# Kernel tuning notes

Hardware: AMD Instinct MI355X
Metric: run time of the kernel (lower is better)

## Reference

```python
import jax, jax.numpy as jnp
import numpy as np

N = 100000      # nodes per protein batch
E = 1600000     # edges per protein batch
F = 128         # num_features_pro
D = 128         # output_dim
B = 128         # number of graphs in the batch
NEG_SLOPE = 0.01  # nn.LeakyReLU default


def setup_inputs() -> dict:
    key = jax.random.key(0)
    ks = jax.random.split(key, 16)
    inp = {}
    inp["pro1_x"] = jax.random.normal(ks[0], (N, F), dtype=jnp.float32)
    inp["pro2_x"] = jax.random.normal(ks[1], (N, F), dtype=jnp.float32)
    inp["pro1_edge_index"] = jax.random.randint(ks[2], (2, E), 0, N, dtype=jnp.int64 if jax.config.jax_enable_x64 else jnp.int32)
    inp["pro2_edge_index"] = jax.random.randint(ks[3], (2, E), 0, N, dtype=jnp.int64 if jax.config.jax_enable_x64 else jnp.int32)
    inp["pro1_batch"] = jnp.sort(jax.random.randint(ks[4], (N,), 0, B))
    inp["pro2_batch"] = jnp.sort(jax.random.randint(ks[5], (N,), 0, B))
    s = 1.0 / np.sqrt(F)
    inp["conv1_W"] = jax.random.uniform(ks[6], (F, D), minval=-s, maxval=s)
    inp["conv1_b"] = jnp.zeros((D,), jnp.float32)
    inp["conv2_W"] = jax.random.uniform(ks[7], (F, D), minval=-s, maxval=s)
    inp["conv2_b"] = jnp.zeros((D,), jnp.float32)
    sd = 1.0 / np.sqrt(D)
    inp["fc_p1_W"] = jax.random.uniform(ks[8], (D, D), minval=-sd, maxval=sd)
    inp["fc_p1_b"] = jax.random.uniform(ks[9], (D,), minval=-sd, maxval=sd)
    inp["fc_p2_W"] = jax.random.uniform(ks[10], (D, D), minval=-sd, maxval=sd)
    inp["fc_p2_b"] = jax.random.uniform(ks[11], (D,), minval=-sd, maxval=sd)
    s1 = 1.0 / np.sqrt(2 * D)
    inp["fc1_W"] = jax.random.uniform(ks[12], (2 * D, 256), minval=-s1, maxval=s1)
    inp["fc1_b"] = jnp.zeros((256,), jnp.float32)
    s2 = 1.0 / np.sqrt(256)
    inp["fc2_W"] = jax.random.uniform(ks[13], (256, 64), minval=-s2, maxval=s2)
    inp["fc2_b"] = jnp.zeros((64,), jnp.float32)
    s3 = 1.0 / np.sqrt(64)
    inp["out_W"] = jax.random.uniform(ks[14], (64, 1), minval=-s3, maxval=s3)
    inp["out_b"] = jnp.zeros((1,), jnp.float32)
    return inp


def lrelu(x):
    return jnp.where(x >= 0, x, NEG_SLOPE * x)


def gcn_conv(x, edge_index, W, b):
    n = x.shape[0]
    xw = x @ W  # [N, D]
    loop = jnp.arange(n, dtype=edge_index.dtype)
    row = jnp.concatenate([edge_index[0], loop])  # sources
    col = jnp.concatenate([edge_index[1], loop])  # destinations
    deg = jax.ops.segment_sum(jnp.ones_like(col, dtype=xw.dtype), col, num_segments=n)
    dinv = jnp.where(deg > 0, jax.lax.rsqrt(deg), 0.0)
    norm = dinv[row] * dinv[col]  # [E+N]
    msg = norm[:, None] * xw[row]  # gather + scale
    return jax.ops.segment_sum(msg, col, num_segments=n) + b


def branch(x, edge_index, batch, conv_W, conv_b, fc_W, fc_b):
    h = lrelu(gcn_conv(x, edge_index, conv_W, conv_b))
    g = jax.ops.segment_max(h, batch, num_segments=B)  # global max pool -> [B, D]
    return lrelu(g @ fc_W + fc_b)  # dropout is identity at eval


def reference(pro1_x, pro1_edge_index, pro1_batch, pro2_x, pro2_edge_index, pro2_batch,
              conv1_W, conv1_b, conv2_W, conv2_b, fc_p1_W, fc_p1_b, fc_p2_W, fc_p2_b,
              fc1_W, fc1_b, fc2_W, fc2_b, out_W, out_b):
    g1 = branch(pro1_x, pro1_edge_index, pro1_batch, conv1_W, conv1_b, fc_p1_W, fc_p1_b)
    g2 = branch(pro2_x, pro2_edge_index, pro2_batch, conv2_W, conv2_b, fc_p2_W, fc_p2_b)
    c = jnp.concatenate([g1, g2], axis=1)  # [B, 2D]
    c = lrelu(c @ fc1_W + fc1_b)
    c = lrelu(c @ fc2_W + fc2_b)
    return jax.nn.sigmoid(c @ out_W + out_b)  # [B, 1]
```

## Files before the change

### kernel.cpp

```cpp
#include <hip/hip_runtime.h>
#include <math.h>

#define NSLOPE 0.01f
#define BGRAPH 128
#define GTILE 128
#define PNB 512
#define MAXBUK 2048
#define SCAP 4608
#define SCHUNK 6400

typedef unsigned int uv4 __attribute__((ext_vector_type(4)));
typedef short bf16x8 __attribute__((ext_vector_type(8)));
typedef float f32x4 __attribute__((ext_vector_type(4)));

__device__ __forceinline__ float lrelu(float v) { return v >= 0.f ? v : NSLOPE * v; }

__device__ __forceinline__ unsigned fkey(float v) {
  v = v + 0.0f;
  unsigned b = __float_as_uint(v);
  return (b & 0x80000000u) ? ~b : (b | 0x80000000u);
}
__device__ __forceinline__ float fdec(unsigned k) {
  return __uint_as_float((k & 0x80000000u) ? (k ^ 0x80000000u) : ~k);
}
__device__ __forceinline__ unsigned bf16rne(float f) {
  unsigned b = __float_as_uint(f);
  return (b + 0x7fffu + ((b >> 16) & 1u)) >> 16;
}
__device__ __forceinline__ void bfunpack8(uint4 w, float4& lo, float4& hi) {
  lo.x = __uint_as_float(w.x << 16); lo.y = __uint_as_float(w.x & 0xffff0000u);
  lo.z = __uint_as_float(w.y << 16); lo.w = __uint_as_float(w.y & 0xffff0000u);
  hi.x = __uint_as_float(w.z << 16); hi.y = __uint_as_float(w.z & 0xffff0000u);
  hi.z = __uint_as_float(w.w << 16); hi.w = __uint_as_float(w.w & 0xffff0000u);
}
__device__ __forceinline__ void add8(float4& alo, float4& ahi, const float4 lo, const float4 hi) {
  alo.x += lo.x; alo.y += lo.y; alo.z += lo.z; alo.w += lo.w;
  ahi.x += hi.x; ahi.y += hi.y; ahi.z += hi.z; ahi.w += hi.w;
}

__global__ __launch_bounds__(1024) void partition_kernel(
    const int* __restrict__ s1, const int* __restrict__ d1,
    const int* __restrict__ s2, const int* __restrict__ d2,
    int* __restrict__ cnt, int* __restrict__ ebuf,
    int ne, int off, int nbuk) {
  __shared__ int h[MAXBUK];
  __shared__ int lbase[MAXBUK + 1];
  __shared__ int cur[MAXBUK];
  __shared__ int sorted[SCHUNK];
  __shared__ int sscan[1024];
  int t = threadIdx.x;
  for (int i = t; i < nbuk; i += 1024) h[i] = 0;
  __syncthreads();
  int total = 2 * ne;
  int chunk = (total + gridDim.x - 1) / gridDim.x;
  int a = blockIdx.x * chunk;
  int b = min(total, a + chunk);
  int m = b - a;
  for (int e = a + t; e < b; e += 1024) {
    int d = (e < ne) ? d1[e] : d2[e - ne] + off;
    atomicAdd(&h[d >> 7], 1);
  }
  __syncthreads();
  int a0 = (2 * t < nbuk) ? h[2 * t] : 0;
  int a1 = (2 * t + 1 < nbuk) ? h[2 * t + 1] : 0;
  int ps = a0 + a1;
  sscan[t] = ps;
  __syncthreads();
  for (int o = 1; o < 1024; o <<= 1) {
    int u = (t >= o) ? sscan[t - o] : 0;
    __syncthreads();
    sscan[t] += u;
    __syncthreads();
  }
  int excl = sscan[t] - ps;
  if (2 * t < nbuk) { lbase[2 * t] = excl; cur[2 * t] = excl; }
  if (2 * t + 1 < nbuk) { lbase[2 * t + 1] = excl + a0; cur[2 * t + 1] = excl + a0; }
  if (t == 0) lbase[nbuk] = sscan[1023];
  __syncthreads();
  for (int i = t; i < nbuk; i += 1024) {
    int hv = h[i];
    if (hv) h[i] = i * SCAP + atomicAdd(&cnt[i], hv) - lbase[i];
  }
  __syncthreads();
  for (int e = a + t; e < b; e += 1024) {
    int s, d;
    if (e < ne) { s = s1[e]; d = d1[e]; }
    else { s = s2[e - ne] + off; d = d2[e - ne] + off; }
    int bk = d >> 7;
    int p = atomicAdd(&cur[bk], 1);
    sorted[p] = (s << 7) | (d & 127);
  }
  __syncthreads();
  for (int i = t; i < m; i += 1024) {
    int lo = 0, hi = nbuk - 1;
    while (lo < hi) {
      int mid = (lo + hi + 1) >> 1;
      if (lbase[mid] <= i) lo = mid; else hi = mid - 1;
    }
    ebuf[h[lo] + i] = sorted[i];
  }
}

__global__ __launch_bounds__(256) void bucket_sort_kernel(
    int* __restrict__ ebuf, const int* __restrict__ cnt,
    int* __restrict__ rowptr, int* __restrict__ rowend, float* __restrict__ dinv,
    const float* __restrict__ x1, const float* __restrict__ x2,
    uint2* __restrict__ xh,
    const float* __restrict__ W1, const float* __restrict__ W2,
    unsigned short* __restrict__ Wt1, unsigned short* __restrict__ Wt2,
    unsigned* __restrict__ gbuf, int n1, int ntot) {
  __shared__ int buf[SCAP];
  __shared__ int outv[SCAP];
  __shared__ int h[128];
  __shared__ int sc[128];
  __shared__ int cur[128];
  __shared__ float sdv[128];
  int b = blockIdx.x, t = threadIdx.x;
  if (b < 64) {
    int idx = b * 256 + t;
    int k = idx >> 7, n = idx & 127;
    Wt1[n * 128 + k] = (unsigned short)bf16rne(W1[idx]);
    Wt2[n * 128 + k] = (unsigned short)bf16rne(W2[idx]);
  }
  if (b < 128) gbuf[b * 256 + t] = 0u;
  int v0 = b * 128;
  int e0 = b * SCAP;
  int cntb = cnt[b];
  if (t < 128) h[t] = 0;
  for (int i = t; i < cntb; i += 256) buf[i] = ebuf[e0 + i];
  __syncthreads();
  for (int i = t; i < cntb; i += 256) atomicAdd(&h[buf[i] & 127], 1);
  __syncthreads();
  if (t < 128) sc[t] = h[t];
  __syncthreads();
  for (int off = 1; off < 128; off <<= 1) {
    int u = (t < 128 && t >= off) ? sc[t - off] : 0;
    __syncthreads();
    if (t < 128) sc[t] += u;
    __syncthreads();
  }
  if (t < 128) {
    int excl = sc[t] - h[t];
    cur[t] = excl;
    float dv = rsqrtf((float)(h[t] + 1));
    sdv[t] = dv;
    int v = v0 + t;
    if (v < ntot) {
      rowptr[v] = e0 + excl;
      rowend[v] = e0 + excl + h[t];
      dinv[v] = dv;
    }
  }
  __syncthreads();
  for (int i = t; i < cntb; i += 256) {
    int p = buf[i];
    int pos = atomicAdd(&cur[p & 127], 1);
    outv[pos] = p >> 7;
  }
  __syncthreads();
  for (int i = t; i < cntb; i += 256) ebuf[e0 + i] = outv[i];
  for (int i = t; i < 128 * 32; i += 256) {
    int nl = i >> 5, l = i & 31;
    int v = v0 + nl;
    if (v >= ntot) break;
    const float4* xr = (v < n1) ? (const float4*)(x1 + (size_t)v * 128)
                                : (const float4*)(x2 + (size_t)(v - n1) * 128);
    float4 xv = xr[l];
    float dv = sdv[nl];
    unsigned b0 = bf16rne(dv * xv.x), b1 = bf16rne(dv * xv.y);
    unsigned b2 = bf16rne(dv * xv.z), b3 = bf16rne(dv * xv.w);
    uint2 w;
    w.x = (b1 << 16) | b0;
    w.y = (b3 << 16) | b2;
    xh[(size_t)v * 32 + l] = w;
  }
}

__global__ __launch_bounds__(256) void gather_kernel(
    const uint4* __restrict__ xh, const int* __restrict__ csr,
    const int* __restrict__ rowptr, const int* __restrict__ rowend,
    const float* __restrict__ dinv,
    uv4* __restrict__ agg16, int vbase, int vlimit) {
  int tid = blockIdx.x * blockDim.x + threadIdx.x;
  int v = vbase + (tid >> 4), l = tid & 15;
  if (v >= vlimit) return;
  float4 a0, a1, b0, b1;
  bfunpack8(xh[(size_t)v * 16 + l], a0, a1);
  b0 = make_float4(0.f, 0.f, 0.f, 0.f); b1 = b0;
  int rs = __builtin_nontemporal_load(&rowptr[v]);
  int re = __builtin_nontemporal_load(&rowend[v]);
  float dv = dinv[v];
  int base = rs;
  int idx0 = rs + l;
  int sown = (idx0 < re) ? __builtin_nontemporal_load(&csr[idx0]) : 0;

#define LD(slot, j) w##slot = xh[(size_t)__shfl(sown, (j), 16) * 16 + l]
#define UP(slot, p0, p1) { float4 lo_, hi_; bfunpack8(w##slot, lo_, hi_); add8(p0, p1, lo_, hi_); }

  for (; base + 16 <= re; base += 16) {
    int nidx = base + 16 + l;
    int snext = (nidx < re) ? __builtin_nontemporal_load(&csr[nidx]) : 0;
    uint4 w0, w1, w2, w3, w4, w5, w6, w7;
    LD(0, 0); LD(1, 1); LD(2, 2); LD(3, 3);
    LD(4, 4); LD(5, 5); LD(6, 6); LD(7, 7);
    UP(0, a0, a1); LD(0, 8);
    UP(1, b0, b1); LD(1, 9);
    UP(2, a0, a1); LD(2, 10);
    UP(3, b0, b1); LD(3, 11);
    UP(4, a0, a1); LD(4, 12);
    UP(5, b0, b1); LD(5, 13);
    UP(6, a0, a1); LD(6, 14);
    UP(7, b0, b1); LD(7, 15);
    UP(0, a0, a1); UP(1, b0, b1); UP(2, a0, a1); UP(3, b0, b1);
    UP(4, a0, a1); UP(5, b0, b1); UP(6, a0, a1); UP(7, b0, b1);
    sown = snext;
  }
  int m = re - base;
  if (m >= 8) {
    uint4 w0, w1, w2, w3, w4, w5, w6, w7;
    LD(0, 0); LD(1, 1); LD(2, 2); LD(3, 3);
    LD(4, 4); LD(5, 5); LD(6, 6); LD(7, 7);
    UP(0, a0, a1); UP(1, b0, b1); UP(2, a0, a1); UP(3, b0, b1);
    UP(4, a0, a1); UP(5, b0, b1); UP(6, a0, a1); UP(7, b0, b1);
  }
  int jb = m & 8;
  int rem = m & 7;
  if (rem) {
    uint4 t0, t1, t2, t3, t4, t5, t6;
    if (rem > 0) t0 = xh[(size_t)__shfl(sown, jb + 0, 16) * 16 + l];
    if (rem > 1) t1 = xh[(size_t)__shfl(sown, jb + 1, 16) * 16 + l];
    if (rem > 2) t2 = xh[(size_t)__shfl(sown, jb + 2, 16) * 16 + l];
    if (rem > 3) t3 = xh[(size_t)__shfl(sown, jb + 3, 16) * 16 + l];
    if (rem > 4) t4 = xh[(size_t)__shfl(sown, jb + 4, 16) * 16 + l];
    if (rem > 5) t5 = xh[(size_t)__shfl(sown, jb + 5, 16) * 16 + l];
    if (rem > 6) t6 = xh[(size_t)__shfl(sown, jb + 6, 16) * 16 + l];
    float4 lo, hi;
    if (rem > 0) { bfunpack8(t0, lo, hi); add8(a0, a1, lo, hi); }
    if (rem > 1) { bfunpack8(t1, lo, hi); add8(b0, b1, lo, hi); }
    if (rem > 2) { bfunpack8(t2, lo, hi); add8(a0, a1, lo, hi); }
    if (rem > 3) { bfunpack8(t3, lo, hi); add8(b0, b1, lo, hi); }
    if (rem > 4) { bfunpack8(t4, lo, hi); add8(a0, a1, lo, hi); }
    if (rem > 5) { bfunpack8(t5, lo, hi); add8(b0, b1, lo, hi); }
    if (rem > 6) { bfunpack8(t6, lo, hi); add8(a0, a1, lo, hi); }
  }
#undef LD
#undef UP

  add8(a0, a1, b0, b1);
  uv4 w;
  w.x = (bf16rne(dv * a0.y) << 16) | bf16rne(dv * a0.x);
  w.y = (bf16rne(dv * a0.w) << 16) | bf16rne(dv * a0.z);
  w.z = (bf16rne(dv * a1.y) << 16) | bf16rne(dv * a1.x);
  w.w = (bf16rne(dv * a1.w) << 16) | bf16rne(dv * a1.z);
  __builtin_nontemporal_store(w, &agg16[(size_t)v * 16 + l]);
}

__global__ __launch_bounds__(256) void gemm_mfma_pool_kernel(
    const bf16x8* __restrict__ A8,
    const bf16x8* __restrict__ Wt1, const float* __restrict__ b1,
    const bf16x8* __restrict__ Wt2, const float* __restrict__ b2,
    const int* __restrict__ batch1, const int* __restrict__ batch2,
    unsigned* __restrict__ gbuf, int N1, int Ntot, int nbA) {
  __shared__ int sgid[128];
  __shared__ unsigned lmax[8 * 128];
  __shared__ int s_span;
  int b = blockIdx.x;
  int half = (b >= nbA) ? 1 : 0;
  const bf16x8* Wt = half ? Wt2 : Wt1;
  const float* bias = half ? b2 : b1;
  int base = half ? (N1 + (b - nbA) * GTILE) : b * GTILE;
  int rmax = half ? Ntot : N1;
  int t = threadIdx.x;
  int w = t >> 6, lane = t & 63;
  int quad = lane >> 4, lr = lane & 15;

  if (t < 128) {
    int gr = base + t;
    int gid = -1;
    if (gr < rmax) gid = half ? (BGRAPH + batch2[gr - N1]) : batch1[gr];
    sgid[t] = gid;
  }
  for (int i = t; i < 8 * 128; i += 256) lmax[i] = 0u;
  __syncthreads();
  int g0 = sgid[0];
  if (t == 0) {
    int mg = g0;
    for (int r = 127; r >= 0; r--) {
      if (sgid[r] >= 0) { mg = sgid[r]; break; }
    }
    s_span = mg - g0 + 1;
  }

  f32x4 acc[2][8];
#pragma unroll
  for (int si = 0; si < 2; si++)
#pragma unroll
    for (int ct = 0; ct < 8; ct++) acc[si][ct] = (f32x4){0.f, 0.f, 0.f, 0.f};

  int r0 = base + w * 16 + lr;
  int r1 = base + (w + 4) * 16 + lr;
#pragma unroll
  for (int kq = 0; kq < 4; kq++) {
    bf16x8 a0 = {0, 0, 0, 0, 0, 0, 0, 0};
    bf16x8 a1 = {0, 0, 0, 0, 0, 0, 0, 0};
    if (r0 < rmax) a0 = A8[(size_t)r0 * 16 + kq * 4 + quad];
    if (r1 < rmax) a1 = A8[(size_t)r1 * 16 + kq * 4 + quad];
#pragma unroll
    for (int ct = 0; ct < 8; ct++) {
      bf16x8 bf = Wt[(size_t)(ct * 16 + lr) * 16 + kq * 4 + quad];
      acc[0][ct] = __builtin_amdgcn_mfma_f32_16x16x32_bf16(a0, bf, acc[0][ct], 0, 0, 0);
      acc[1][ct] = __builtin_amdgcn_mfma_f32_16x16x32_bf16(a1, bf, acc[1][ct], 0, 0, 0);
    }
  }

  float bv[8];
#pragma unroll
  for (int ct = 0; ct < 8; ct++) bv[ct] = bias[ct * 16 + lr];
#pragma unroll
  for (int si = 0; si < 2; si++) {
    int slab = (si == 0) ? w : (w + 4);
#pragma unroll
    for (int reg = 0; reg < 4; reg++) {
      int rl = slab * 16 + quad * 4 + reg;
      int gid = sgid[rl];
      if (gid < 0) continue;
      int loc = gid - g0;
#pragma unroll
      for (int ct = 0; ct < 8; ct++) {
        unsigned key = fkey(lrelu(acc[si][ct][reg] + bv[ct]));
        if (loc < 8) atomicMax(&lmax[loc * 128 + ct * 16 + lr], key);
        else atomicMax(&gbuf[(size_t)gid * 128 + ct * 16 + lr], key);
      }
    }
  }
  __syncthreads();
  int span = s_span; if (span > 8) span = 8;
  for (int i = t; i < span * 128; i += 256) {
    unsigned k = lmax[i];
    if (k) atomicMax(&gbuf[(size_t)(g0 + (i >> 7)) * 128 + (i & 127)], k);
  }
}


__global__ __launch_bounds__(256) void head_kernel(
    const unsigned* __restrict__ gbuf,
    const float* __restrict__ fcp1W, const float* __restrict__ fcp1b,
    const float* __restrict__ fcp2W, const float* __restrict__ fcp2b,
    const float* __restrict__ fc1W, const float* __restrict__ fc1b,
    const float* __restrict__ fc2W, const float* __restrict__ fc2b,
    const float* __restrict__ outW, const float* __restrict__ outb,
    float* __restrict__ out) {
  __shared__ float grow[256];
  __shared__ float c[256];
  __shared__ float h1[256];
  __shared__ float h2[64];
  int b = blockIdx.x, t = threadIdx.x;
  grow[t] = (t < 128) ? fdec(gbuf[(size_t)b * 128 + t])
                      : fdec(gbuf[(size_t)(BGRAPH + b) * 128 + (t - 128)]);
  __syncthreads();
  {
    float acc;
    if (t < 128) {
      acc = fcp1b[t];
      for (int k = 0; k < 128; k++) acc = fmaf(grow[k], fcp1W[k * 128 + t], acc);
    } else {
      int tc = t - 128;
      acc = fcp2b[tc];
      for (int k = 0; k < 128; k++) acc = fmaf(grow[128 + k], fcp2W[k * 128 + tc], acc);
    }
    c[t] = lrelu(acc);
  }
  __syncthreads();
  {
    float acc = fc1b[t];
    for (int k = 0; k < 256; k++) acc = fmaf(c[k], fc1W[k * 256 + t], acc);
    h1[t] = lrelu(acc);
  }
  __syncthreads();
  if (t < 64) {
    float acc = fc2b[t];
    for (int k = 0; k < 256; k++) acc = fmaf(h1[k], fc2W[k * 64 + t], acc);
    h2[t] = lrelu(acc);
  }
  __syncthreads();
  if (t < 64) {
    float v = h2[t] * outW[t];
    for (int off = 32; off > 0; off >>= 1) v += __shfl_down(v, off);
    if (t == 0) out[b] = 1.f / (1.f + expf(-(v + outb[0])));
  }
}

extern "C" void kernel_launch(void* const* d_in, const int* in_sizes, int n_in,
                              void* d_out, int out_size, void* d_ws, size_t ws_size,
                              hipStream_t stream) {
  const float* x1 = (const float*)d_in[0];
  const float* x2 = (const float*)d_in[1];
  const int* ei1 = (const int*)d_in[2];
  const int* ei2 = (const int*)d_in[3];
  const int* batch1 = (const int*)d_in[4];
  const int* batch2 = (const int*)d_in[5];
  const float* conv1W = (const float*)d_in[6];
  const float* conv1b = (const float*)d_in[7];
  const float* conv2W = (const float*)d_in[8];
  const float* conv2b = (const float*)d_in[9];
  const float* fcp1W = (const float*)d_in[10];
  const float* fcp1b = (const float*)d_in[11];
  const float* fcp2W = (const float*)d_in[12];
  const float* fcp2b = (const float*)d_in[13];
  const float* fc1W = (const float*)d_in[14];
  const float* fc1b = (const float*)d_in[15];
  const float* fc2W = (const float*)d_in[16];
  const float* fc2b = (const float*)d_in[17];
  const float* outW = (const float*)d_in[18];
  const float* outb = (const float*)d_in[19];

  int N = in_sizes[0] / 128;
  int E = in_sizes[2] / 2;
  int NT = 2 * N;
  int NBUK = (NT + 127) / 128;

  char* ws = (char*)d_ws;
  size_t off = 0;
  auto alloc = [&](size_t bytes) -> void* {
    void* p = ws + off;
    off += (bytes + 511) & ~(size_t)511;
    return p;
  };
  uint2* xh = (uint2*)alloc((size_t)NT * 256);
  uint2* agg16 = (uint2*)alloc((size_t)NT * 256);
  int* ebuf = (int*)alloc((size_t)NBUK * SCAP * 4);
  int* rowptr = (int*)alloc((size_t)NT * 4);
  int* rowend = (int*)alloc((size_t)NT * 4);
  float* dinv = (float*)alloc((size_t)NT * 4);
  int* cnt = (int*)alloc((size_t)NBUK * 4);
  unsigned* gbuf = (unsigned*)alloc((size_t)2 * BGRAPH * 128 * 4);
  unsigned short* Wt1 = (unsigned short*)alloc((size_t)128 * 128 * 2);
  unsigned short* Wt2 = (unsigned short*)alloc((size_t)128 * 128 * 2);
  (void)ws_size; (void)n_in; (void)out_size;

  const int* src1 = ei1, *dst1 = ei1 + E;
  const int* src2 = ei2, *dst2 = ei2 + E;

  hipMemsetAsync(cnt, 0, (size_t)NBUK * 4, stream);
  partition_kernel<<<PNB, 1024, 0, stream>>>(src1, dst1, src2, dst2, cnt, ebuf, E, N, NBUK);
  bucket_sort_kernel<<<NBUK, 256, 0, stream>>>(ebuf, cnt, rowptr, rowend, dinv,
                                               x1, x2, xh, conv1W, conv2W, Wt1, Wt2,
                                               gbuf, N, NT);
  int half = (NT / 2 + 127) & ~127;
  gather_kernel<<<(unsigned)(((size_t)half * 16 + 255) / 256), 256, 0, stream>>>(
      (const uint4*)xh, ebuf, rowptr, rowend, dinv, (uv4*)agg16, 0, half);
  gather_kernel<<<(unsigned)(((size_t)(NT - half) * 16 + 255) / 256), 256, 0, stream>>>(
      (const uint4*)xh, ebuf, rowptr, rowend, dinv, (uv4*)agg16, half, NT);
  int nbA = (N + GTILE - 1) / GTILE;
  gemm_mfma_pool_kernel<<<2 * nbA, 256, 0, stream>>>(
      (const bf16x8*)agg16, (const bf16x8*)Wt1, conv1b, (const bf16x8*)Wt2, conv2b,
      batch1, batch2, gbuf, N, NT, nbA);
  head_kernel<<<BGRAPH, 256, 0, stream>>>(gbuf, fcp1W, fcp1b, fcp2W, fcp2b,
                                          fc1W, fc1b, fc2W, fc2b, outW, outb,
                                          (float*)d_out);
}
```

Baseline: 412.3 us.

## Stage weights in swizzled LDS and pre-reduce same-graph rows before pooling atomics

Copies the 128x128 bf16 weight tile into LDS with an XOR swizzle instead of each wave reading it from global memory, and prefetches A fragments before the barrier. In the pooling epilogue, when a quad's four rows share a graph id, it takes the max in registers first and issues one atomic instead of four. It also replaces the serial span scan by thread 0 with a direct lookup of the last valid row. The 32KB of LDS may lower occupancy.

```diff
diff --git a/kernel.cpp b/kernel.cpp
--- a/kernel.cpp
+++ b/kernel.cpp
@@ -263,10 +263,10 @@
     unsigned* __restrict__ gbuf, int N1, int Ntot, int nbA) {
   __shared__ int sgid[128];
   __shared__ unsigned lmax[8 * 128];
-  __shared__ int s_span;
+  __shared__ uint4 wtile[128 * 16];
   int b = blockIdx.x;
   int half = (b >= nbA) ? 1 : 0;
-  const bf16x8* Wt = half ? Wt2 : Wt1;
+  const uint4* Wt = (const uint4*)(half ? Wt2 : Wt1);
   const float* bias = half ? b2 : b1;
   int base = half ? (N1 + (b - nbA) * GTILE) : b * GTILE;
   int rmax = half ? Ntot : N1;
@@ -281,60 +281,78 @@
     sgid[t] = gid;
   }
   for (int i = t; i < 8 * 128; i += 256) lmax[i] = 0u;
-  __syncthreads();
-  int g0 = sgid[0];
-  if (t == 0) {
-    int mg = g0;
-    for (int r = 127; r >= 0; r--) {
-      if (sgid[r] >= 0) { mg = sgid[r]; break; }
-    }
-    s_span = mg - g0 + 1;
-  }
-
-  f32x4 acc[2][8];
-#pragma unroll
-  for (int si = 0; si < 2; si++)
-#pragma unroll
-    for (int ct = 0; ct < 8; ct++) acc[si][ct] = (f32x4){0.f, 0.f, 0.f, 0.f};
+  for (int i = t; i < 2048; i += 256) {
+    int row = i >> 4, q = i & 15;
+    wtile[(row << 4) | (q ^ (row & 7))] = Wt[i];
+  }
 
   int r0 = base + w * 16 + lr;
   int r1 = base + (w + 4) * 16 + lr;
+  bf16x8 af0[4], af1[4];
 #pragma unroll
   for (int kq = 0; kq < 4; kq++) {
-    bf16x8 a0 = {0, 0, 0, 0, 0, 0, 0, 0};
-    bf16x8 a1 = {0, 0, 0, 0, 0, 0, 0, 0};
-    if (r0 < rmax) a0 = A8[(size_t)r0 * 16 + kq * 4 + quad];
-    if (r1 < rmax) a1 = A8[(size_t)r1 * 16 + kq * 4 + quad];
+    af0[kq] = (bf16x8){0, 0, 0, 0, 0, 0, 0, 0};
+    af1[kq] = (bf16x8){0, 0, 0, 0, 0, 0, 0, 0};
+    if (r0 < rmax) af0[kq] = ((const bf16x8*)A8)[(size_t)r0 * 16 + kq * 4 + quad];
+    if (r1 < rmax) af1[kq] = ((const bf16x8*)A8)[(size_t)r1 * 16 + kq * 4 + quad];
+  }
+  __syncthreads();
+
+  f32x4 acc[2][8];
+#pragma unroll
+  for (int si = 0; si < 2; si++)
+#pragma unroll
+    for (int ct = 0; ct < 8; ct++) acc[si][ct] = (f32x4){0.f, 0.f, 0.f, 0.f};
+
+#pragma unroll
+  for (int kq = 0; kq < 4; kq++) {
+    int q = kq * 4 + quad;
 #pragma unroll
     for (int ct = 0; ct < 8; ct++) {
-      bf16x8 bf = Wt[(size_t)(ct * 16 + lr) * 16 + kq * 4 + quad];
-      acc[0][ct] = __builtin_amdgcn_mfma_f32_16x16x32_bf16(a0, bf, acc[0][ct], 0, 0, 0);
-      acc[1][ct] = __builtin_amdgcn_mfma_f32_16x16x32_bf16(a1, bf, acc[1][ct], 0, 0, 0);
+      bf16x8 bf = *(const bf16x8*)&wtile[((ct * 16 + lr) << 4) | (q ^ (lr & 7))];
+      acc[0][ct] = __builtin_amdgcn_mfma_f32_16x16x32_bf16(af0[kq], bf, acc[0][ct], 0, 0, 0);
+      acc[1][ct] = __builtin_amdgcn_mfma_f32_16x16x32_bf16(af1[kq], bf, acc[1][ct], 0, 0, 0);
     }
   }
 
+  int g0 = sgid[0];
   float bv[8];
 #pragma unroll
   for (int ct = 0; ct < 8; ct++) bv[ct] = bias[ct * 16 + lr];
 #pragma unroll
   for (int si = 0; si < 2; si++) {
     int slab = (si == 0) ? w : (w + 4);
-#pragma unroll
-    for (int reg = 0; reg < 4; reg++) {
-      int rl = slab * 16 + quad * 4 + reg;
-      int gid = sgid[rl];
-      if (gid < 0) continue;
-      int loc = gid - g0;
+    int rb = slab * 16 + quad * 4;
+    int ga = sgid[rb], gz = sgid[rb + 3];
+    if (ga == gz) {
+      if (ga < 0) continue;
+      int loc = ga - g0;
 #pragma unroll
       for (int ct = 0; ct < 8; ct++) {
-        unsigned key = fkey(lrelu(acc[si][ct][reg] + bv[ct]));
+        f32x4 v = acc[si][ct];
+        float mx = fmaxf(fmaxf(v[0], v[1]), fmaxf(v[2], v[3]));
+        unsigned key = fkey(lrelu(mx + bv[ct]));
         if (loc < 8) atomicMax(&lmax[loc * 128 + ct * 16 + lr], key);
-        else atomicMax(&gbuf[(size_t)gid * 128 + ct * 16 + lr], key);
+        else atomicMax(&gbuf[(size_t)ga * 128 + ct * 16 + lr], key);
+      }
+    } else {
+#pragma unroll
+      for (int reg = 0; reg < 4; reg++) {
+        int gid = sgid[rb + reg];
+        if (gid < 0) continue;
+        int loc = gid - g0;
+#pragma unroll
+        for (int ct = 0; ct < 8; ct++) {
+          unsigned key = fkey(lrelu(acc[si][ct][reg] + bv[ct]));
+          if (loc < 8) atomicMax(&lmax[loc * 128 + ct * 16 + lr], key);
+          else atomicMax(&gbuf[(size_t)gid * 128 + ct * 16 + lr], key);
+        }
       }
     }
   }
   __syncthreads();
-  int span = s_span; if (span > 8) span = 8;
+  int lastv = rmax - base - 1; if (lastv > 127) lastv = 127;
+  int span = sgid[lastv] - g0 + 1; if (span > 8) span = 8;
   for (int i = t; i < span * 128; i += 256) {
     unsigned k = lmax[i];
     if (k) atomicMax(&gbuf[(size_t)(g0 + (i >> 7)) * 128 + (i & 127)], k);
```

Measured after the change: 390.5 us. -5.3%, faster.
